# Optimization experiments

Measured on AMD Instinct MI355X. Metric: run time of the kernel, lower is better.

The kernel has to match this reference:

```python
import jax, jax.numpy as jnp
import numpy as np

B, HDIM, H, W = 1, 256, 48, 48
KDIM = 2048
TOP = int(0.1 * KDIM)  # 204, matches int(0.1*self.k)


def _l2norm(v):
    # matches torch F.normalize(dim=1, eps=1e-12)
    return v / jnp.maximum(jnp.linalg.norm(v, axis=1, keepdims=True), 1e-12)


def setup_inputs() -> dict:
    key = jax.random.key(0)
    k1, k2, k3 = jax.random.split(key, 3)
    return {
        "x": jax.random.normal(k1, (B, HDIM, H, W), dtype=jnp.float32),
        "feat_units": jax.random.normal(k2, (KDIM, HDIM), dtype=jnp.float32),
        "label_units": jax.random.normal(k3, (KDIM, 4), dtype=jnp.float32),
    }


def reference(x, feat_units, label_units):
    # update_flag='topk', y=None path of MemoryN2N.forward
    b, c, h, w = x.shape
    xf = x.transpose(0, 2, 3, 1).reshape(-1, c)          # (n, c)
    score = _l2norm(xf) @ _l2norm(feat_units).T           # (n, k) cosine scores
    weight = jax.nn.softmax(score, axis=1)                # (n, k)
    # torch.sort(descending)[1][:, :TOP] == top_k indices (same values)
    _, top_idx = jax.lax.top_k(score, TOP)                # (n, TOP) int32
    sel_wt = jnp.take_along_axis(weight, top_idx, axis=1)  # (n, TOP)
    out_x = jnp.einsum('nk,nkc->nc', sel_wt, feat_units[top_idx])   # (n, c)
    out_y = jnp.einsum('nk,nkc->nc', sel_wt, label_units[top_idx])  # (n, 4)

    def to_img(t, ch):
        return t.reshape(b, h, w, ch).transpose(0, 3, 1, 2)

    out = jnp.concatenate([x, to_img(out_x, c), to_img(out_y, 4)], axis=1)  # (b, 2c+4, h, w)
    return out, score
```

## Files before the change

kernel.cpp:

```cpp
#include <hip/hip_runtime.h>
#include <math.h>

#define N_PIX 2304
#define CDIM  256
#define KDIM  2048
#define TOPK  204

typedef __attribute__((ext_vector_type(8))) short bf16x8;
typedef __attribute__((ext_vector_type(4))) float f32x4;

__device__ __forceinline__ unsigned short f2bf(float f) {
    unsigned u = __float_as_uint(f);
    unsigned r = u + 0x7FFFu + ((u >> 16) & 1u);
    return (unsigned short)(r >> 16);
}

__device__ __forceinline__ void gload16(const void* g, void* l) {
    __builtin_amdgcn_global_load_lds((const __attribute__((address_space(1))) void*)g,
                                     (__attribute__((address_space(3))) void*)l,
                                     16, 0, 0);
}

__global__ __launch_bounds__(256) void k_prep(const float* __restrict__ x,
                                              const float* __restrict__ feat,
                                              const float* __restrict__ label,
                                              float* __restrict__ out,
                                              unsigned short* __restrict__ xn,
                                              unsigned short* __restrict__ fnorm,
                                              unsigned short* __restrict__ F2T) {
    __shared__ __align__(16) char sm[68608];
    int b = blockIdx.x, t = threadIdx.x;

    if (b < 36) {
        float* tile  = (float*)sm;
        float* part  = (float*)(sm + 66560);
        float* rnloc = (float*)(sm + 67584);
        int p0 = b * 64;
        #pragma unroll
        for (int i = 0; i < 64; ++i) {
            int idx = t + i * 256;
            int c = idx >> 6, pl = idx & 63;
            float v = x[c * N_PIX + p0 + pl];
            tile[c * 65 + pl] = v;
            out[c * N_PIX + p0 + pl] = v;
        }
        __syncthreads();
        {
            int pixel = t & 63, q = t >> 6;
            float s = 0.f;
            #pragma unroll
            for (int i = 0; i < 64; ++i) {
                float v = tile[(q * 64 + i) * 65 + pixel];
                s = fmaf(v, v, s);
            }
            part[q * 64 + pixel] = s;
        }
        __syncthreads();
        if (t < 64) {
            float tt = part[t] + part[64 + t] + part[128 + t] + part[192 + t];
            rnloc[t] = 1.0f / fmaxf(sqrtf(tt), 1e-12f);
        }
        __syncthreads();
        {
            int p = t >> 2, cq = t & 3;
            float rn = rnloc[p];
            #pragma unroll
            for (int j = 0; j < 8; ++j) {
                bf16x8 pk;
                #pragma unroll
                for (int jj = 0; jj < 8; ++jj)
                    pk[jj] = (short)f2bf(tile[(cq * 64 + j * 8 + jj) * 65 + p] * rn);
                *(bf16x8*)(xn + (size_t)(p0 + p) * CDIM + cq * 64 + j * 8) = pk;
            }
        }
    } else {
        float* tile = (float*)sm;
        int r0 = (b - 36) * 64;
        #pragma unroll
        for (int i = 0; i < 64; ++i) {
            int idx = t + i * 256;
            int r = idx >> 8, c = idx & 255;
            tile[r * 257 + c] = feat[(size_t)(r0 + r) * CDIM + c];
        }
        __syncthreads();
        int row = t >> 2, q = t & 3;
        float s = 0.f;
        #pragma unroll
        for (int i = 0; i < 64; ++i) {
            float v = tile[row * 257 + q * 64 + i];
            s = fmaf(v, v, s);
        }
        s += __shfl_xor(s, 1, 64);
        s += __shfl_xor(s, 2, 64);
        float rn = 1.0f / fmaxf(sqrtf(s), 1e-12f);
        #pragma unroll
        for (int j = 0; j < 8; ++j) {
            bf16x8 pk;
            #pragma unroll
            for (int jj = 0; jj < 8; ++jj)
                pk[jj] = (short)f2bf(tile[row * 257 + q * 64 + j * 8 + jj] * rn);
            *(bf16x8*)(fnorm + (size_t)(r0 + row) * CDIM + q * 64 + j * 8) = pk;
        }
        __syncthreads();
        {
            int rp = (t & 31) * 2, cg = t >> 5;
            #pragma unroll
            for (int i = 0; i < 32; ++i) {
                int c = i * 8 + cg;
                unsigned u0 = f2bf(tile[rp * 257 + c]);
                unsigned u1 = f2bf(tile[(rp + 1) * 257 + c]);
                *(unsigned*)(F2T + (size_t)c * KDIM + r0 + rp) = u0 | (u1 << 16);
            }
        }
        {
            int ch = t >> 6, r = t & 63;
            F2T[(size_t)(256 + ch) * KDIM + r0 + r] = f2bf(label[(size_t)(r0 + r) * 4 + ch]);
        }
        #pragma unroll
        for (int i = 0; i < 15; ++i) {
            int idx = t + i * 256;
            int zr = idx >> 6, zc = idx & 63;
            F2T[(size_t)(260 + zr) * KDIM + r0 + zc] = 0;
        }
    }
}

__global__ __launch_bounds__(256) void k_gemm1(const unsigned short* __restrict__ A,
                                               const unsigned short* __restrict__ B,
                                               float* __restrict__ C) {
    __shared__ __align__(16) unsigned short smA[2][128 * 32];
    __shared__ __align__(16) unsigned short smB[2][128 * 32];
    int t = threadIdx.x, l = t & 63, w = t >> 6;
    int m0 = blockIdx.y * 128, n0 = blockIdx.x * 128;
    int wr = w >> 1, wc = w & 1;

    f32x4 acc[4][4] = {};

    #pragma unroll
    for (int r = 0; r < 2; ++r) {
        int row = r * 64 + w * 16 + (l >> 2);
        int ch  = (l & 3) ^ ((row >> 1) & 3);
        gload16(A + (size_t)(m0 + row) * CDIM + ch * 8, &smA[0][(r * 64 + w * 16) * 32]);
        gload16(B + (size_t)(n0 + row) * CDIM + ch * 8, &smB[0][(r * 64 + w * 16) * 32]);
    }
    __syncthreads();

    for (int ks = 0; ks < 8; ++ks) {
        int cur = ks & 1;
        if (ks < 7) {
            int k0 = (ks + 1) * 32;
            #pragma unroll
            for (int r = 0; r < 2; ++r) {
                int row = r * 64 + w * 16 + (l >> 2);
                int ch  = (l & 3) ^ ((row >> 1) & 3);
                gload16(A + (size_t)(m0 + row) * CDIM + k0 + ch * 8, &smA[cur ^ 1][(r * 64 + w * 16) * 32]);
                gload16(B + (size_t)(n0 + row) * CDIM + k0 + ch * 8, &smB[cur ^ 1][(r * 64 + w * 16) * 32]);
            }
        }
        bf16x8 av[4], bv[4];
        #pragma unroll
        for (int mi = 0; mi < 4; ++mi) {
            int R = wr * 64 + mi * 16 + (l & 15);
            av[mi] = *(const bf16x8*)&smA[cur][R * 32 + (((l >> 4) ^ ((R >> 1) & 3)) << 3)];
        }
        #pragma unroll
        for (int ni = 0; ni < 4; ++ni) {
            int R = wc * 64 + ni * 16 + (l & 15);
            bv[ni] = *(const bf16x8*)&smB[cur][R * 32 + (((l >> 4) ^ ((R >> 1) & 3)) << 3)];
        }
        #pragma unroll
        for (int mi = 0; mi < 4; ++mi)
            #pragma unroll
            for (int ni = 0; ni < 4; ++ni)
                acc[mi][ni] = __builtin_amdgcn_mfma_f32_16x16x32_bf16(av[mi], bv[ni], acc[mi][ni], 0, 0, 0);
        __syncthreads();
    }

    #pragma unroll
    for (int mi = 0; mi < 4; ++mi)
        #pragma unroll
        for (int ni = 0; ni < 4; ++ni) {
            int rbase = m0 + wr * 64 + mi * 16 + (l >> 4) * 4;
            int cidx  = n0 + wc * 64 + ni * 16 + (l & 15);
            #pragma unroll
            for (int r = 0; r < 4; ++r)
                C[(size_t)(rbase + r) * KDIM + cidx] = acc[mi][ni][r];
        }
}

__global__ __launch_bounds__(256) void k_select(const float* __restrict__ score,
                                                unsigned short* __restrict__ Wm) {
    int t = threadIdx.x, l = t & 63, w = t >> 6;
    int row = blockIdx.x * 4 + w;
    const float* srow = score + (size_t)row * KDIM;

    float s[32];
    #pragma unroll
    for (int j = 0; j < 8; ++j) {
        float4 v = *(const float4*)(srow + j * 256 + l * 4);
        s[j * 4 + 0] = v.x; s[j * 4 + 1] = v.y; s[j * 4 + 2] = v.z; s[j * 4 + 3] = v.w;
    }

    float d = 0.f;
    #pragma unroll
    for (int j = 0; j < 32; ++j) d += __expf(s[j]);
    #pragma unroll
    for (int off = 32; off; off >>= 1) d += __shfl_xor(d, off, 64);
    float rd = 1.0f / d;

    float lo = -1.5f, hi = 1.5f;
    #pragma unroll 1
    for (int it = 0; it < 22; ++it) {
        float mid = 0.5f * (lo + hi);
        int c = 0;
        #pragma unroll
        for (int j = 0; j < 32; ++j) c += (s[j] > mid) ? 1 : 0;
        #pragma unroll
        for (int off = 32; off; off >>= 1) c += __shfl_xor(c, off, 64);
        if (c >= TOPK) lo = mid; else hi = mid;
    }

    #pragma unroll
    for (int j = 0; j < 8; ++j) {
        ushort4 pk;
        pk.x = (s[j*4+0] > lo) ? f2bf(__expf(s[j*4+0]) * rd) : (unsigned short)0;
        pk.y = (s[j*4+1] > lo) ? f2bf(__expf(s[j*4+1]) * rd) : (unsigned short)0;
        pk.z = (s[j*4+2] > lo) ? f2bf(__expf(s[j*4+2]) * rd) : (unsigned short)0;
        pk.w = (s[j*4+3] > lo) ? f2bf(__expf(s[j*4+3]) * rd) : (unsigned short)0;
        *(ushort4*)(Wm + (size_t)row * KDIM + j * 256 + l * 4) = pk;
    }
}

__global__ __launch_bounds__(256) void k_gemm2(const unsigned short* __restrict__ W,
                                               const unsigned short* __restrict__ F2T,
                                               float* __restrict__ out) {
    __shared__ __align__(16) char sm[65536];
    int t = threadIdx.x, l = t & 63, w = t >> 6;
    int m0 = blockIdx.y * 64, n0 = blockIdx.x * 64;
    char* wbase = sm + w * 16384;
    int   kb    = w * 512;

    f32x4 acc[4][4] = {};

    #pragma unroll
    for (int i = 0; i < 4; ++i) {
        int row = i * 16 + (l >> 2);
        int ch  = (l & 3) ^ ((row >> 1) & 3);
        gload16(W   + (size_t)(m0 + row) * KDIM + kb + ch * 8, wbase + i * 1024);
        gload16(F2T + (size_t)(n0 + row) * KDIM + kb + ch * 8, wbase + 8192 + i * 1024);
    }

    for (int ks = 0; ks < 16; ++ks) {
        int cur = ks & 1;
        if (ks < 15) {
            int koff = kb + (ks + 1) * 32;
            #pragma unroll
            for (int i = 0; i < 4; ++i) {
                int row = i * 16 + (l >> 2);
                int ch  = (l & 3) ^ ((row >> 1) & 3);
                gload16(W   + (size_t)(m0 + row) * KDIM + koff + ch * 8, wbase + (cur ^ 1) * 4096 + i * 1024);
                gload16(F2T + (size_t)(n0 + row) * KDIM + koff + ch * 8, wbase + 8192 + (cur ^ 1) * 4096 + i * 1024);
            }
            asm volatile("s_waitcnt vmcnt(8)" ::: "memory");
        } else {
            asm volatile("s_waitcnt vmcnt(0)" ::: "memory");
        }
        bf16x8 av[4], bv[4];
        #pragma unroll
        for (int mi = 0; mi < 4; ++mi) {
            int R = mi * 16 + (l & 15);
            av[mi] = *(const bf16x8*)(wbase + cur * 4096 + R * 64 + (((l >> 4) ^ ((R >> 1) & 3)) << 4));
        }
        #pragma unroll
        for (int ni = 0; ni < 4; ++ni) {
            int R = ni * 16 + (l & 15);
            bv[ni] = *(const bf16x8*)(wbase + 8192 + cur * 4096 + R * 64 + (((l >> 4) ^ ((R >> 1) & 3)) << 4));
        }
        #pragma unroll
        for (int mi = 0; mi < 4; ++mi)
            #pragma unroll
            for (int ni = 0; ni < 4; ++ni)
                acc[mi][ni] = __builtin_amdgcn_mfma_f32_16x16x32_bf16(av[mi], bv[ni], acc[mi][ni], 0, 0, 0);
    }

    __syncthreads();
    float* tl = (float*)sm;
    if (w >= 2) {
        float* dst = tl + (w - 2) * 64 * 65;
        #pragma unroll
        for (int mi = 0; mi < 4; ++mi)
            #pragma unroll
            for (int ni = 0; ni < 4; ++ni) {
                int rr = mi * 16 + (l >> 4) * 4;
                int cc = ni * 16 + (l & 15);
                #pragma unroll
                for (int r = 0; r < 4; ++r)
                    dst[(rr + r) * 65 + cc] = acc[mi][ni][r];
            }
    }
    __syncthreads();
    if (w < 2) {
        float* dst = tl + w * 64 * 65;
        #pragma unroll
        for (int mi = 0; mi < 4; ++mi)
            #pragma unroll
            for (int ni = 0; ni < 4; ++ni) {
                int rr = mi * 16 + (l >> 4) * 4;
                int cc = ni * 16 + (l & 15);
                #pragma unroll
                for (int r = 0; r < 4; ++r)
                    dst[(rr + r) * 65 + cc] += acc[mi][ni][r];
            }
    }
    __syncthreads();
    int pl = t & 63, cg = t >> 6;
    #pragma unroll
    for (int i = 0; i < 16; ++i) {
        int cc = cg * 16 + i;
        int c_out = n0 + cc;
        int orow;
        if (c_out < 256) orow = 256 + c_out;
        else if (c_out < 260) orow = 512 + (c_out - 256);
        else continue;
        out[(size_t)orow * N_PIX + m0 + pl] = tl[pl * 65 + cc] + tl[64 * 65 + pl * 65 + cc];
    }
}

extern "C" void kernel_launch(void* const* d_in, const int* in_sizes, int n_in,
                              void* d_out, int out_size, void* d_ws, size_t ws_size,
                              hipStream_t stream) {
    const float* x     = (const float*)d_in[0];
    const float* feat  = (const float*)d_in[1];
    const float* label = (const float*)d_in[2];
    float* out   = (float*)d_out;
    float* score = out + 516 * N_PIX;

    char* ws = (char*)d_ws;
    unsigned short* xn    = (unsigned short*)(ws);
    unsigned short* fnorm = (unsigned short*)(ws + 1179648);
    unsigned short* F2T   = (unsigned short*)(ws + 2228224);
    unsigned short* Wm    = (unsigned short*)(ws + 3538944);

    k_prep  <<<68,           256, 0, stream>>>(x, feat, label, out, xn, fnorm, F2T);
    k_gemm1 <<<dim3(16, 18), 256, 0, stream>>>(xn, fnorm, score);
    k_select<<<576,          256, 0, stream>>>(score, Wm);
    k_gemm2 <<<dim3(5, 36),  256, 0, stream>>>(Wm, F2T, out);
}
```

Before: 57.47 us.

## Fuse four kernels into one cooperative persistent kernel with grid syncs

Merges the prep, score GEMM, top-k select, and output GEMM stages into a single cooperative kernel of 288 blocks separated by grid-wide syncs, so there is one launch instead of four. The select stage now handles two rows per wave so the grid size stays fixed. The prep stage keeps its shared-memory tile in bf16 instead of fp32 so it fits in the shared 64KB buffer. This removes inter-kernel launch gaps, at the cost of grid-sync overhead and possible occupancy limits from the merged register and shared-memory footprint. A fallback to four separate launches is kept in case the cooperative launch fails.

```diff
diff --git a/kernel.cpp b/kernel.cpp
--- a/kernel.cpp
+++ b/kernel.cpp
@@ -1,5 +1,8 @@
 #include <hip/hip_runtime.h>
+#include <hip/hip_cooperative_groups.h>
 #include <math.h>
+
+namespace cg = cooperative_groups;
 
 #define N_PIX 2304
 #define CDIM  256
@@ -14,6 +17,9 @@
     unsigned r = u + 0x7FFFu + ((u >> 16) & 1u);
     return (unsigned short)(r >> 16);
 }
+__device__ __forceinline__ float bf2f(unsigned short h) {
+    return __uint_as_float((unsigned)h << 16);
+}
 
 __device__ __forceinline__ void gload16(const void* g, void* l) {
     __builtin_amdgcn_global_load_lds((const __attribute__((address_space(1))) void*)g,
@@ -21,28 +27,26 @@
                                      16, 0, 0);
 }
 
-__global__ __launch_bounds__(256) void k_prep(const float* __restrict__ x,
-                                              const float* __restrict__ feat,
-                                              const float* __restrict__ label,
-                                              float* __restrict__ out,
-                                              unsigned short* __restrict__ xn,
-                                              unsigned short* __restrict__ fnorm,
-                                              unsigned short* __restrict__ F2T) {
-    __shared__ __align__(16) char sm[68608];
-    int b = blockIdx.x, t = threadIdx.x;
-
+__device__ __forceinline__ void ph_prep(int b, int t, char* sm,
+                                        const float* __restrict__ x,
+                                        const float* __restrict__ feat,
+                                        const float* __restrict__ label,
+                                        float* __restrict__ out,
+                                        unsigned short* __restrict__ xn,
+                                        unsigned short* __restrict__ fnorm,
+                                        unsigned short* __restrict__ F2T) {
     if (b < 36) {
-        float* tile  = (float*)sm;
-        float* part  = (float*)(sm + 66560);
-        float* rnloc = (float*)(sm + 67584);
+        unsigned short* tile = (unsigned short*)sm;
+        float* part  = (float*)(sm + 33792);
+        float* rnloc = (float*)(sm + 34816);
         int p0 = b * 64;
         #pragma unroll
         for (int i = 0; i < 64; ++i) {
             int idx = t + i * 256;
             int c = idx >> 6, pl = idx & 63;
             float v = x[c * N_PIX + p0 + pl];
-            tile[c * 65 + pl] = v;
             out[c * N_PIX + p0 + pl] = v;
+            tile[c * 66 + pl] = f2bf(v);
         }
         __syncthreads();
         {
@@ -50,7 +54,7 @@
             float s = 0.f;
             #pragma unroll
             for (int i = 0; i < 64; ++i) {
-                float v = tile[(q * 64 + i) * 65 + pixel];
+                float v = bf2f(tile[(q * 64 + i) * 66 + pixel]);
                 s = fmaf(v, v, s);
             }
             part[q * 64 + pixel] = s;
@@ -69,25 +73,22 @@
                 bf16x8 pk;
                 #pragma unroll
                 for (int jj = 0; jj < 8; ++jj)
-                    pk[jj] = (short)f2bf(tile[(cq * 64 + j * 8 + jj) * 65 + p] * rn);
+                    pk[jj] = (short)f2bf(bf2f(tile[(cq * 64 + j * 8 + jj) * 66 + p]) * rn);
                 *(bf16x8*)(xn + (size_t)(p0 + p) * CDIM + cq * 64 + j * 8) = pk;
             }
         }
     } else {
-        float* tile = (float*)sm;
+        unsigned short* tile = (unsigned short*)sm;
         int r0 = (b - 36) * 64;
         #pragma unroll
-        for (int i = 0; i < 64; ++i) {
-            int idx = t + i * 256;
-            int r = idx >> 8, c = idx & 255;
-            tile[r * 257 + c] = feat[(size_t)(r0 + r) * CDIM + c];
-        }
+        for (int i = 0; i < 64; ++i)
+            tile[i * 264 + t] = f2bf(feat[(size_t)(r0 + i) * CDIM + t]);
         __syncthreads();
         int row = t >> 2, q = t & 3;
         float s = 0.f;
         #pragma unroll
         for (int i = 0; i < 64; ++i) {
-            float v = tile[row * 257 + q * 64 + i];
+            float v = bf2f(tile[row * 264 + q * 64 + i]);
             s = fmaf(v, v, s);
         }
         s += __shfl_xor(s, 1, 64);
@@ -98,17 +99,17 @@
             bf16x8 pk;
             #pragma unroll
             for (int jj = 0; jj < 8; ++jj)
-                pk[jj] = (short)f2bf(tile[row * 257 + q * 64 + j * 8 + jj] * rn);
+                pk[jj] = (short)f2bf(bf2f(tile[row * 264 + q * 64 + j * 8 + jj]) * rn);
             *(bf16x8*)(fnorm + (size_t)(r0 + row) * CDIM + q * 64 + j * 8) = pk;
         }
         __syncthreads();
         {
-            int rp = (t & 31) * 2, cg = t >> 5;
+            int rp = (t & 31) * 2, cg2 = t >> 5;
             #pragma unroll
             for (int i = 0; i < 32; ++i) {
-                int c = i * 8 + cg;
-                unsigned u0 = f2bf(tile[rp * 257 + c]);
-                unsigned u1 = f2bf(tile[(rp + 1) * 257 + c]);
+                int c = i * 8 + cg2;
+                unsigned u0 = tile[rp * 264 + c];
+                unsigned u1 = tile[(rp + 1) * 264 + c];
                 *(unsigned*)(F2T + (size_t)c * KDIM + r0 + rp) = u0 | (u1 << 16);
             }
         }
@@ -125,13 +126,14 @@
     }
 }
 
-__global__ __launch_bounds__(256) void k_gemm1(const unsigned short* __restrict__ A,
-                                               const unsigned short* __restrict__ B,
-                                               float* __restrict__ C) {
-    __shared__ __align__(16) unsigned short smA[2][128 * 32];
-    __shared__ __align__(16) unsigned short smB[2][128 * 32];
-    int t = threadIdx.x, l = t & 63, w = t >> 6;
-    int m0 = blockIdx.y * 128, n0 = blockIdx.x * 128;
+__device__ __forceinline__ void ph_gemm1(int b, int t, char* smraw,
+                                         const unsigned short* __restrict__ A,
+                                         const unsigned short* __restrict__ B,
+                                         float* __restrict__ C) {
+    unsigned short* smA = (unsigned short*)smraw;
+    unsigned short* smB = (unsigned short*)(smraw + 16384);
+    int l = t & 63, w = t >> 6;
+    int m0 = (b >> 4) * 128, n0 = (b & 15) * 128;
     int wr = w >> 1, wc = w & 1;
 
     f32x4 acc[4][4] = {};
@@ -140,8 +142,8 @@
     for (int r = 0; r < 2; ++r) {
         int row = r * 64 + w * 16 + (l >> 2);
         int ch  = (l & 3) ^ ((row >> 1) & 3);
-        gload16(A + (size_t)(m0 + row) * CDIM + ch * 8, &smA[0][(r * 64 + w * 16) * 32]);
-        gload16(B + (size_t)(n0 + row) * CDIM + ch * 8, &smB[0][(r * 64 + w * 16) * 32]);
+        gload16(A + (size_t)(m0 + row) * CDIM + ch * 8, &smA[(r * 64 + w * 16) * 32]);
+        gload16(B + (size_t)(n0 + row) * CDIM + ch * 8, &smB[(r * 64 + w * 16) * 32]);
     }
     __syncthreads();
 
@@ -153,20 +155,22 @@
             for (int r = 0; r < 2; ++r) {
                 int row = r * 64 + w * 16 + (l >> 2);
                 int ch  = (l & 3) ^ ((row >> 1) & 3);
-                gload16(A + (size_t)(m0 + row) * CDIM + k0 + ch * 8, &smA[cur ^ 1][(r * 64 + w * 16) * 32]);
-                gload16(B + (size_t)(n0 + row) * CDIM + k0 + ch * 8, &smB[cur ^ 1][(r * 64 + w * 16) * 32]);
+                gload16(A + (size_t)(m0 + row) * CDIM + k0 + ch * 8,
+                        &smA[(cur ^ 1) * 4096 + (r * 64 + w * 16) * 32]);
+                gload16(B + (size_t)(n0 + row) * CDIM + k0 + ch * 8,
+                        &smB[(cur ^ 1) * 4096 + (r * 64 + w * 16) * 32]);
             }
         }
         bf16x8 av[4], bv[4];
         #pragma unroll
         for (int mi = 0; mi < 4; ++mi) {
             int R = wr * 64 + mi * 16 + (l & 15);
-            av[mi] = *(const bf16x8*)&smA[cur][R * 32 + (((l >> 4) ^ ((R >> 1) & 3)) << 3)];
+            av[mi] = *(const bf16x8*)&smA[cur * 4096 + R * 32 + (((l >> 4) ^ ((R >> 1) & 3)) << 3)];
         }
         #pragma unroll
         for (int ni = 0; ni < 4; ++ni) {
             int R = wc * 64 + ni * 16 + (l & 15);
-            bv[ni] = *(const bf16x8*)&smB[cur][R * 32 + (((l >> 4) ^ ((R >> 1) & 3)) << 3)];
+            bv[ni] = *(const bf16x8*)&smB[cur * 4096 + R * 32 + (((l >> 4) ^ ((R >> 1) & 3)) << 3)];
         }
         #pragma unroll
         for (int mi = 0; mi < 4; ++mi)
@@ -188,55 +192,59 @@
         }
 }
 
-__global__ __launch_bounds__(256) void k_select(const float* __restrict__ score,
-                                                unsigned short* __restrict__ Wm) {
-    int t = threadIdx.x, l = t & 63, w = t >> 6;
-    int row = blockIdx.x * 4 + w;
-    const float* srow = score + (size_t)row * KDIM;
-
-    float s[32];
-    #pragma unroll
-    for (int j = 0; j < 8; ++j) {
-        float4 v = *(const float4*)(srow + j * 256 + l * 4);
-        s[j * 4 + 0] = v.x; s[j * 4 + 1] = v.y; s[j * 4 + 2] = v.z; s[j * 4 + 3] = v.w;
-    }
-
-    float d = 0.f;
-    #pragma unroll
-    for (int j = 0; j < 32; ++j) d += __expf(s[j]);
-    #pragma unroll
-    for (int off = 32; off; off >>= 1) d += __shfl_xor(d, off, 64);
-    float rd = 1.0f / d;
-
-    float lo = -1.5f, hi = 1.5f;
+__device__ __forceinline__ void ph_select(int b, int t,
+                                          const float* __restrict__ score,
+                                          unsigned short* __restrict__ Wm) {
+    int l = t & 63, w = t >> 6;
     #pragma unroll 1
-    for (int it = 0; it < 22; ++it) {
-        float mid = 0.5f * (lo + hi);
-        int c = 0;
-        #pragma unroll
-        for (int j = 0; j < 32; ++j) c += (s[j] > mid) ? 1 : 0;
-        #pragma unroll
-        for (int off = 32; off; off >>= 1) c += __shfl_xor(c, off, 64);
-        if (c >= TOPK) lo = mid; else hi = mid;
-    }
-
-    #pragma unroll
-    for (int j = 0; j < 8; ++j) {
-        ushort4 pk;
-        pk.x = (s[j*4+0] > lo) ? f2bf(__expf(s[j*4+0]) * rd) : (unsigned short)0;
-        pk.y = (s[j*4+1] > lo) ? f2bf(__expf(s[j*4+1]) * rd) : (unsigned short)0;
-        pk.z = (s[j*4+2] > lo) ? f2bf(__expf(s[j*4+2]) * rd) : (unsigned short)0;
-        pk.w = (s[j*4+3] > lo) ? f2bf(__expf(s[j*4+3]) * rd) : (unsigned short)0;
-        *(ushort4*)(Wm + (size_t)row * KDIM + j * 256 + l * 4) = pk;
-    }
-}
-
-__global__ __launch_bounds__(256) void k_gemm2(const unsigned short* __restrict__ W,
-                                               const unsigned short* __restrict__ F2T,
-                                               float* __restrict__ out) {
-    __shared__ __align__(16) char sm[65536];
-    int t = threadIdx.x, l = t & 63, w = t >> 6;
-    int m0 = blockIdx.y * 64, n0 = blockIdx.x * 64;
+    for (int rr = 0; rr < 2; ++rr) {
+        int row = b * 8 + w * 2 + rr;
+        const float* srow = score + (size_t)row * KDIM;
+
+        float s[32];
+        #pragma unroll
+        for (int j = 0; j < 8; ++j) {
+            float4 v = *(const float4*)(srow + j * 256 + l * 4);
+            s[j * 4 + 0] = v.x; s[j * 4 + 1] = v.y; s[j * 4 + 2] = v.z; s[j * 4 + 3] = v.w;
+        }
+
+        float d = 0.f;
+        #pragma unroll
+        for (int j = 0; j < 32; ++j) d += __expf(s[j]);
+        #pragma unroll
+        for (int off = 32; off; off >>= 1) d += __shfl_xor(d, off, 64);
+        float rd = 1.0f / d;
+
+        float lo = -1.5f, hi = 1.5f;
+        #pragma unroll 1
+        for (int it = 0; it < 22; ++it) {
+            float mid = 0.5f * (lo + hi);
+            int c = 0;
+            #pragma unroll
+            for (int j = 0; j < 32; ++j) c += (s[j] > mid) ? 1 : 0;
+            #pragma unroll
+            for (int off = 32; off; off >>= 1) c += __shfl_xor(c, off, 64);
+            if (c >= TOPK) lo = mid; else hi = mid;
+        }
+
+        #pragma unroll
+        for (int j = 0; j < 8; ++j) {
+            ushort4 pk;
+            pk.x = (s[j*4+0] > lo) ? f2bf(__expf(s[j*4+0]) * rd) : (unsigned short)0;
+            pk.y = (s[j*4+1] > lo) ? f2bf(__expf(s[j*4+1]) * rd) : (unsigned short)0;
+            pk.z = (s[j*4+2] > lo) ? f2bf(__expf(s[j*4+2]) * rd) : (unsigned short)0;
+            pk.w = (s[j*4+3] > lo) ? f2bf(__expf(s[j*4+3]) * rd) : (unsigned short)0;
+            *(ushort4*)(Wm + (size_t)row * KDIM + j * 256 + l * 4) = pk;
+        }
+    }
+}
+
+__device__ __forceinline__ void ph_gemm2(int b, int t, char* sm,
+                                         const unsigned short* __restrict__ W,
+                                         const unsigned short* __restrict__ F2T,
+                                         float* __restrict__ out) {
+    int l = t & 63, w = t >> 6;
+    int m0 = (b / 5) * 64, n0 = (b % 5) * 64;
     char* wbase = sm + w * 16384;
     int   kb    = w * 512;
 
@@ -291,11 +299,11 @@
         for (int mi = 0; mi < 4; ++mi)
             #pragma unroll
             for (int ni = 0; ni < 4; ++ni) {
-                int rr = mi * 16 + (l >> 4) * 4;
-                int cc = ni * 16 + (l & 15);
+                int rr2 = mi * 16 + (l >> 4) * 4;
+                int cc  = ni * 16 + (l & 15);
                 #pragma unroll
                 for (int r = 0; r < 4; ++r)
-                    dst[(rr + r) * 65 + cc] = acc[mi][ni][r];
+                    dst[(rr2 + r) * 65 + cc] = acc[mi][ni][r];
             }
     }
     __syncthreads();
@@ -305,18 +313,18 @@
         for (int mi = 0; mi < 4; ++mi)
             #pragma unroll
             for (int ni = 0; ni < 4; ++ni) {
-                int rr = mi * 16 + (l >> 4) * 4;
-                int cc = ni * 16 + (l & 15);
+                int rr2 = mi * 16 + (l >> 4) * 4;
+                int cc  = ni * 16 + (l & 15);
                 #pragma unroll
                 for (int r = 0; r < 4; ++r)
-                    dst[(rr + r) * 65 + cc] += acc[mi][ni][r];
+                    dst[(rr2 + r) * 65 + cc] += acc[mi][ni][r];
             }
     }
     __syncthreads();
-    int pl = t & 63, cg = t >> 6;
+    int pl = t & 63, cg2 = t >> 6;
     #pragma unroll
     for (int i = 0; i < 16; ++i) {
-        int cc = cg * 16 + i;
+        int cc = cg2 * 16 + i;
         int c_out = n0 + cc;
         int orow;
         if (c_out < 256) orow = 256 + c_out;
@@ -324,6 +332,46 @@
         else continue;
         out[(size_t)orow * N_PIX + m0 + pl] = tl[pl * 65 + cc] + tl[64 * 65 + pl * 65 + cc];
     }
+}
+
+__global__ __launch_bounds__(256, 2) void k_mega(const float* __restrict__ x,
+                                                 const float* __restrict__ feat,
+                                                 const float* __restrict__ label,
+                                                 float* __restrict__ out,
+                                                 unsigned short* __restrict__ xn,
+                                                 unsigned short* __restrict__ fnorm,
+                                                 unsigned short* __restrict__ F2T,
+                                                 unsigned short* __restrict__ Wm,
+                                                 float* __restrict__ score) {
+    __shared__ __align__(16) char sm[65536];
+    int b = blockIdx.x, t = threadIdx.x;
+    cg::grid_group grid = cg::this_grid();
+
+    if (b < 68) ph_prep(b, t, sm, x, feat, label, out, xn, fnorm, F2T);
+    grid.sync();
+    ph_gemm1(b, t, sm, xn, fnorm, score);
+    grid.sync();
+    ph_select(b, t, score, Wm);
+    grid.sync();
+    if (b < 180) ph_gemm2(b, t, sm, Wm, F2T, out);
+}
+
+__global__ __launch_bounds__(256) void k_prep_f(const float* x, const float* feat, const float* label,
+                                                float* out, unsigned short* xn, unsigned short* fnorm,
+                                                unsigned short* F2T) {
+    __shared__ __align__(16) char sm[36864];
+    ph_prep(blockIdx.x, threadIdx.x, sm, x, feat, label, out, xn, fnorm, F2T);
+}
+__global__ __launch_bounds__(256) void k_gemm1_f(const unsigned short* A, const unsigned short* B, float* C) {
+    __shared__ __align__(16) char sm[32768];
+    ph_gemm1(blockIdx.x, threadIdx.x, sm, A, B, C);
+}
+__global__ __launch_bounds__(256) void k_select_f(const float* score, unsigned short* Wm) {
+    ph_select(blockIdx.x, threadIdx.x, score, Wm);
+}
+__global__ __launch_bounds__(256) void k_gemm2_f(const unsigned short* W, const unsigned short* F2T, float* out) {
+    __shared__ __align__(16) char sm[65536];
+    ph_gemm2(blockIdx.x, threadIdx.x, sm, W, F2T, out);
 }
 
 extern "C" void kernel_launch(void* const* d_in, const int* in_sizes, int n_in,
@@ -341,8 +389,15 @@
     unsigned short* F2T   = (unsigned short*)(ws + 2228224);
     unsigned short* Wm    = (unsigned short*)(ws + 3538944);
 
-    k_prep  <<<68,           256, 0, stream>>>(x, feat, label, out, xn, fnorm, F2T);
-    k_gemm1 <<<dim3(16, 18), 256, 0, stream>>>(xn, fnorm, score);
-    k_select<<<576,          256, 0, stream>>>(score, Wm);
-    k_gemm2 <<<dim3(5, 36),  256, 0, stream>>>(Wm, F2T, out);
-}
+    void* args[] = {(void*)&x, (void*)&feat, (void*)&label, (void*)&out,
+                    (void*)&xn, (void*)&fnorm, (void*)&F2T, (void*)&Wm, (void*)&score};
+    hipError_t e = hipLaunchCooperativeKernel((const void*)k_mega, dim3(288), dim3(256),
+                                              args, 0, stream);
+    if (e != hipSuccess) {
+        (void)hipGetLastError();
+        k_prep_f  <<<68,  256, 0, stream>>>(x, feat, label, out, xn, fnorm, F2T);
+        k_gemm1_f <<<288, 256, 0, stream>>>(xn, fnorm, score);
+        k_select_f<<<288, 256, 0, stream>>>(score, Wm);
+        k_gemm2_f <<<180, 256, 0, stream>>>(Wm, F2T, out);
+    }
+}
```

After: 171.8 us. +198.9%, slower.
